# Kernel optimization log

Measured on AMD Instinct MI355X. Metric: run time of the kernel, lower is better.

The kernel has to match this reference:

```python
import jax, jax.numpy as jnp
import numpy as np

B, T, D, H, OUT, VOCAB = 64, 100, 1024, 1024, 28, 28


def setup_inputs() -> dict:
    key = jax.random.key(0)
    ks = jax.random.split(key, 12)
    s = 0.05
    return {
        "x": jax.random.normal(ks[0], (B, T, D), jnp.float32),
        # encoder GRU (keras reset_after=True): kernel [D,3H], recurrent [H,3H], bias [2,3H]
        "enc_W": jax.random.normal(ks[1], (D, 3 * H), jnp.float32) * s,
        "enc_U": jax.random.normal(ks[2], (H, 3 * H), jnp.float32) * s,
        "enc_b": jax.random.normal(ks[3], (2, 3 * H), jnp.float32) * s,
        # AdditiveAttention learned scale vector [H]
        "att_scale": jax.random.normal(ks[4], (H,), jnp.float32) * s,
        # Embedding(28, H)
        "emb_W": jax.random.normal(ks[5], (VOCAB, H), jnp.float32) * s,
        # decoder GRUCell
        "dec_W": jax.random.normal(ks[6], (H, 3 * H), jnp.float32) * s,
        "dec_U": jax.random.normal(ks[7], (H, 3 * H), jnp.float32) * s,
        "dec_b": jax.random.normal(ks[8], (2, 3 * H), jnp.float32) * s,
        # fc: Dense(OUT) on concat([h, context]) -> [2H, OUT]
        "fc_W": jax.random.normal(ks[9], (2 * H, OUT), jnp.float32) * s,
        "fc_b": jax.random.normal(ks[10], (OUT,), jnp.float32) * s,
    }


def _gru_update(x_t, h, W, U, b):
    # keras GRU math with reset_after=True
    mx = x_t @ W + b[0]          # [B,3H]
    mi = h @ U + b[1]            # [B,3H]
    xz, xr, xh = jnp.split(mx, 3, axis=-1)
    rz, rr, rh = jnp.split(mi, 3, axis=-1)
    z = jax.nn.sigmoid(xz + rz)
    r = jax.nn.sigmoid(xr + rr)
    hh = jnp.tanh(xh + r * rh)
    return z * h + (1.0 - z) * hh


def reference(x, enc_W, enc_U, enc_b, att_scale, emb_W, dec_W, dec_U, dec_b, fc_W, fc_b):
    b, t, _ = x.shape
    h = jnp.zeros((b, enc_U.shape[0]), x.dtype)

    # encoder GRU, return_sequences=True
    def enc_step(h, x_t):
        h = _gru_update(x_t, h, enc_W, enc_U, enc_b)
        return h, h

    _, hpe = jax.lax.scan(enc_step, h, jnp.swapaxes(x, 0, 1))  # [T,B,H]
    hpe = jnp.swapaxes(hpe, 0, 1)                              # [B,T,H]

    out_dim = fc_b.shape[0]
    p0 = jnp.zeros((b, out_dim), x.dtype)
    h0 = jnp.zeros((b, dec_U.shape[0]), x.dtype)

    def dec_step(carry, _):
        p, hd = carry
        # additive attention: scores[b,j] = sum_d scale[d]*tanh(q[b,d]+k[b,j,d])
        scores = jnp.einsum('bth,h->bt', jnp.tanh(hd[:, None, :] + hpe), att_scale)
        attn = jax.nn.softmax(scores, axis=-1)
        ctx = jnp.einsum('bt,bth->bh', attn, hpe)
        idx = jnp.argmax(p, axis=-1)          # [B] int
        e = emb_W[idx]                        # [B,H]
        hd = _gru_update(e, hd, dec_W, dec_U, dec_b)
        p = jnp.concatenate([hd, ctx], axis=1) @ fc_W + fc_b
        return (p, hd), p

    _, outs = jax.lax.scan(dec_step, (p0, h0), None, length=t)  # [T,B,OUT]
    return jnp.swapaxes(outs, 0, 1)                              # [B,T,OUT]
```

## Files before the change

### kernel.cpp

```cpp
#include <hip/hip_runtime.h>

#define TT 100
#define HH 1024
#define H3 3072
#define NOUT 28

#define AGENT __HIP_MEMORY_SCOPE_AGENT
#define WGRP  __HIP_MEMORY_SCOPE_WORKGROUP
#define SPIN_CAP (1u<<20)

__device__ __forceinline__ float frcp_(float x){ return __builtin_amdgcn_rcpf(x); }
__device__ __forceinline__ float fsig_(float x){ return frcp_(1.0f + __expf(-x)); }
__device__ __forceinline__ float ftanh_(float x){ return 1.0f - 2.0f*frcp_(__expf(2.0f*x) + 1.0f); }
__device__ __forceinline__ void wait_vm(){ asm volatile("s_waitcnt vmcnt(0)" ::: "memory"); }

__device__ __forceinline__ float4 ld_dev16(const float* p){
    float4 v;
    asm volatile("global_load_dwordx4 %0, %1, off sc0 sc1" : "=v"(v) : "v"(p) : "memory");
    return v;
}
__device__ __forceinline__ unsigned aload4(const int* p){
    return (unsigned)__hip_atomic_load(p, __ATOMIC_RELAXED, AGENT);
}

__device__ __forceinline__ void gridbar(int* slot, int sub, int target){
    __syncthreads();
    if (threadIdx.x == 0){
        __hip_atomic_fetch_add(slot + sub*16, 1, __ATOMIC_RELAXED, AGENT);
        unsigned gy = 0; int s;
        do {
            s = 0;
            #pragma unroll
            for (int c=0;c<16;c++) s += __hip_atomic_load(slot + c*16, __ATOMIC_RELAXED, AGENT);
            if (s < target){ if (++gy > SPIN_CAP) break; __builtin_amdgcn_s_sleep(1); }
        } while (s < target);
    }
    __syncthreads();
}

__device__ __forceinline__ void wbar4(int* c, int tgt){
    asm volatile("s_waitcnt lgkmcnt(0)" ::: "memory");
    if ((threadIdx.x & 63) == 0) __hip_atomic_fetch_add(c, 1, __ATOMIC_RELAXED, WGRP);
    unsigned gy = 0;
    while (__hip_atomic_load(c, __ATOMIC_RELAXED, WGRP) < tgt){ if (++gy > SPIN_CAP) break; }
    asm volatile("" ::: "memory");
}

__global__ void k_init(int* ib, int n){
    int g = blockIdx.x*256 + threadIdx.x;
    if (g < n) ib[g] = 0;
}

__global__ __launch_bounds__(256) void k_transpose(const float* __restrict__ U0,
                                                   const float* __restrict__ U1,
                                                   float* __restrict__ T0,
                                                   float* __restrict__ T1){
    const float* U = blockIdx.z ? U1 : U0;
    float*       T = blockIdx.z ? T1 : T0;
    __shared__ float tile[32][33];
    int tx = threadIdx.x & 31, ty = threadIdx.x >> 5;
    int j0 = blockIdx.x*32, k0 = blockIdx.y*32;
    #pragma unroll
    for (int q=0;q<4;q++){
        int kr = ty + q*8;
        tile[kr][tx] = U[(size_t)(k0+kr)*H3 + j0 + tx];
    }
    __syncthreads();
    #pragma unroll
    for (int q=0;q<4;q++){
        int jr = ty + q*8;
        T[(size_t)(j0+jr)*HH + k0 + tx] = tile[tx][jr];
    }
}

__global__ __launch_bounds__(256) void k_edec(const float* __restrict__ emb,
                                              const float* __restrict__ W,
                                              const float* __restrict__ b0,
                                              float* __restrict__ E){
    int gid = blockIdx.x*256 + threadIdx.x;
    int v = gid / H3, j = gid - v*H3;
    float acc = b0[j];
    const float* er = emb + (size_t)v*HH;
    #pragma unroll 4
    for (int k=0;k<HH;k++) acc = fmaf(er[k], W[(size_t)k*H3 + j], acc);
    E[gid] = acc;
}

__global__ __launch_bounds__(256) void k_mxgemm(const float* __restrict__ A,
                                                const float* __restrict__ W,
                                                const float* __restrict__ b0,
                                                float* __restrict__ MXT){
    __shared__ float aT[32*68];
    __shared__ float bL[32*68];
    int tid = threadIdx.x;
    int row0 = blockIdx.y*64, col0 = blockIdx.x*64;
    int arow = tid>>2, acs = (tid&3)*4;
    int bk   = tid>>3, bcs = (tid&7)*4;
    int ty = tid>>4, tx = tid&15;
    float acc[4][4] = {};
    for (int kk=0; kk<HH; kk+=32){
        #pragma unroll
        for (int i=0;i<2;i++){
            int c = acs + i*16;
            float4 v = *(const float4*)(A + (size_t)(row0+arow)*HH + kk + c);
            aT[(c+0)*68 + arow] = v.x; aT[(c+1)*68 + arow] = v.y;
            aT[(c+2)*68 + arow] = v.z; aT[(c+3)*68 + arow] = v.w;
        }
        #pragma unroll
        for (int i=0;i<2;i++){
            int c = bcs + i*32;
            float4 v = *(const float4*)(W + (size_t)(kk+bk)*H3 + col0 + c);
            *(float4*)(bL + bk*68 + c) = v;
        }
        __syncthreads();
        #pragma unroll
        for (int k=0;k<32;k++){
            float4 a4 = *(const float4*)(aT + k*68 + ty*4);
            float4 b4 = *(const float4*)(bL + k*68 + tx*4);
            acc[0][0]=fmaf(a4.x,b4.x,acc[0][0]); acc[0][1]=fmaf(a4.x,b4.y,acc[0][1]);
            acc[0][2]=fmaf(a4.x,b4.z,acc[0][2]); acc[0][3]=fmaf(a4.x,b4.w,acc[0][3]);
            acc[1][0]=fmaf(a4.y,b4.x,acc[1][0]); acc[1][1]=fmaf(a4.y,b4.y,acc[1][1]);
            acc[1][2]=fmaf(a4.y,b4.z,acc[1][2]); acc[1][3]=fmaf(a4.y,b4.w,acc[1][3]);
            acc[2][0]=fmaf(a4.z,b4.x,acc[2][0]); acc[2][1]=fmaf(a4.z,b4.y,acc[2][1]);
            acc[2][2]=fmaf(a4.z,b4.z,acc[2][2]); acc[2][3]=fmaf(a4.z,b4.w,acc[2][3]);
            acc[3][0]=fmaf(a4.w,b4.x,acc[3][0]); acc[3][1]=fmaf(a4.w,b4.y,acc[3][1]);
            acc[3][2]=fmaf(a4.w,b4.z,acc[3][2]); acc[3][3]=fmaf(a4.w,b4.w,acc[3][3]);
        }
        __syncthreads();
    }
    float4 bb = *(const float4*)(b0 + col0 + tx*4);
    #pragma unroll
    for (int i=0;i<4;i++){
        int r = row0 + ty*4 + i;
        int bq = r / 100; int tq = r - bq*100;
        float v0 = acc[i][0] + bb.x, v1 = acc[i][1] + bb.y;
        float v2 = acc[i][2] + bb.z, v3 = acc[i][3] + bb.w;
        float* dst = MXT + ((size_t)tq*H3 + col0 + tx*4)*64 + bq;
        dst[0]   = v0; dst[64]  = v1; dst[128] = v2; dst[192] = v3;
    }
}

__global__ __launch_bounds__(256) void k_enc(const float* __restrict__ MXT,
                                             const float* __restrict__ Ut,
                                             const float* __restrict__ b1,
                                             float* __restrict__ hpe,
                                             float* __restrict__ hT,
                                             int* __restrict__ bar){
    __shared__ float hs[2][16384];
    int tid = threadIdx.x, lane = tid & 63;
    int wg = blockIdx.x;
    int sub = wg & 15;
    int cu = __builtin_amdgcn_readfirstlane(wg*4 + (tid>>6));
    const float* Uz = Ut + (size_t)cu*HH;
    const float* Ur = Uz + (size_t)HH*HH;
    const float* Uh = Ur + (size_t)HH*HH;
    float bz = b1[cu], br = b1[cu+HH], bh = b1[cu+2*HH];
    for (int t=0; t<TT; ++t){
        int cur = t & 1;
        const float* mx = MXT + (size_t)t*H3*64;
        float xz = mx[(size_t)cu*64 + lane];
        float xr = mx[(size_t)(cu+HH)*64 + lane];
        float xh = mx[(size_t)(cu+2*HH)*64 + lane];
        float az=0.f, ar=0.f, ah=0.f, hp=0.f;
        if (t > 0){
            const float* gq = hT + (size_t)cur*65536;
            float4 sv[16];
            #pragma unroll
            for (int s=0;s<16;s++) sv[s] = ld_dev16(gq + 4*(size_t)(s*256 + tid));
            wait_vm();
            #pragma unroll
            for (int s=0;s<16;s++) ((float4*)hs[0])[s*256 + tid] = sv[s];
            __syncthreads();
            for (int q=0;q<4;++q){
                if (q<3){
                    #pragma unroll
                    for (int s=0;s<16;s++) sv[s] = ld_dev16(gq + (size_t)(q+1)*16384 + 4*(size_t)(s*256 + tid));
                }
                const float* hb = hs[q&1];
                const float* Uzq = Uz + q*256;
                const float* Urq = Ur + q*256;
                const float* Uhq = Uh + q*256;
                #pragma unroll 8
                for (int k=0;k<256;++k){
                    float h = hb[k*64 + lane];
                    az = fmaf(h, Uzq[k], az);
                    ar = fmaf(h, Urq[k], ar);
                    ah = fmaf(h, Uhq[k], ah);
                }
                if ((cu>>8) == q) hp = hb[(cu&255)*64 + lane];
                if (q<3){
                    wait_vm();
                    #pragma unroll
                    for (int s=0;s<16;s++) ((float4*)hs[(q+1)&1])[s*256 + tid] = sv[s];
                }
                __syncthreads();
            }
        }
        float z  = fsig_(xz + az + bz);
        float r  = fsig_(xr + ar + br);
        float hh = ftanh_(xh + r*(ah + bh));
        float hnew = z*hp + (1.f - z)*hh;
        __hip_atomic_store(hT + (size_t)(cur^1)*65536 + cu*64 + lane, hnew, __ATOMIC_RELAXED, AGENT);
        hpe[((size_t)lane*TT + t)*HH + cu] = hnew;
        gridbar(bar + (size_t)t*256, sub, 256);
    }
}

__global__ __launch_bounds__(512) void k_dec(const float* __restrict__ hpe,
                                             const float* __restrict__ Ut,
                                             const float* __restrict__ b1,
                                             const float* __restrict__ Edec,
                                             const float* __restrict__ scale,
                                             const float* __restrict__ fcW,
                                             const float* __restrict__ fcb,
                                             float* __restrict__ hdT,
                                             float* __restrict__ hdl,
                                             float* __restrict__ out,
                                             int* __restrict__ idx_t,
                                             int* __restrict__ bar,
                                             int* __restrict__ flagidx){
    __shared__ float hs[2][16384];
    __shared__ float ctxs[4][1024];
    __shared__ float m_s[4], S_s[4];
    __shared__ int c_a, c_fc, go, cstg;
    int tid = threadIdx.x, wg = blockIdx.x;
    if (tid == 0){ c_a=0; c_fc=0; go=0; cstg=0; }
    __syncthreads();

    if (tid < 256){
        int lane = tid & 63;
        int sub = wg & 15;
        int cu = __builtin_amdgcn_readfirstlane(wg*4 + (tid>>6));
        const float* Uz = Ut + (size_t)cu*HH;
        const float* Ur = Uz + (size_t)HH*HH;
        const float* Uh = Ur + (size_t)HH*HH;
        float bz = b1[cu], br = b1[cu+HH], bh = b1[cu+2*HH];
        int stgt = 0;
        for (int i=0; i<TT; ++i){
            int cur = i & 1;
            float az=0.f, ar=0.f, ah=0.f, hp=0.f;
            if (i > 0){
                const float* gq = hdT + (size_t)cur*65536;
                float4 sv[16];
                #pragma unroll
                for (int s=0;s<16;s++) sv[s] = ld_dev16(gq + 4*(size_t)(s*256 + tid));
                wait_vm();
                #pragma unroll
                for (int s=0;s<16;s++) ((float4*)hs[0])[s*256 + tid] = sv[s];
                wbar4(&cstg, stgt += 4);
                for (int q=0;q<4;++q){
                    if (q<3){
                        #pragma unroll
                        for (int s=0;s<16;s++) sv[s] = ld_dev16(gq + (size_t)(q+1)*16384 + 4*(size_t)(s*256 + tid));
                    }
                    const float* hb = hs[q&1];
                    const float* Uzq = Uz + q*256;
                    const float* Urq = Ur + q*256;
                    const float* Uhq = Uh + q*256;
                    #pragma unroll 8
                    for (int k=0;k<256;++k){
                        float h = hb[k*64 + lane];
                        az = fmaf(h, Uzq[k], az);
                        ar = fmaf(h, Urq[k], ar);
                        ah = fmaf(h, Uhq[k], ah);
                    }
                    if ((cu>>8) == q) hp = hb[(cu&255)*64 + lane];
                    if (q<3){
                        wait_vm();
                        #pragma unroll
                        for (int s=0;s<16;s++) ((float4*)hs[(q+1)&1])[s*256 + tid] = sv[s];
                    }
                    wbar4(&cstg, stgt += 4);
                }
            }
            if (tid == 0){
                unsigned gy = 0; int s;
                do {
                    s = 0;
                    #pragma unroll
                    for (int c=0;c<8;c++) s += __hip_atomic_load(flagidx + (size_t)i*128 + c*16, __ATOMIC_RELAXED, AGENT);
                    if (s < 64){ if (++gy > SPIN_CAP) break; __builtin_amdgcn_s_sleep(1); }
                } while (s < 64);
                __hip_atomic_store(&go, i+1, __ATOMIC_RELAXED, WGRP);
            }
            { unsigned gy=0; while (__hip_atomic_load(&go, __ATOMIC_RELAXED, WGRP) < i+1){ if (++gy > SPIN_CAP) break; } }
            asm volatile("" ::: "memory");
            unsigned mi = aload4(idx_t + (size_t)i*64 + lane);
            if (mi > 27u) mi = 0;
            const float* ed = Edec + (size_t)mi*H3;
            float xz = ed[cu], xr = ed[cu+HH], xh = ed[cu+2*HH];
            float z  = fsig_(xz + az + bz);
            float r  = fsig_(xr + ar + br);
            float hh = ftanh_(xh + r*(ah + bh));
            float hnew = z*hp + (1.f - z)*hh;
            __hip_atomic_store(hdT + (size_t)(cur^1)*65536 + cu*64 + lane, hnew, __ATOMIC_RELAXED, AGENT);
            __hip_atomic_store(hdl + (size_t)(cur^1)*65536 + (size_t)lane*HH + cu, hnew, __ATOMIC_RELAXED, AGENT);
            gridbar(bar + (size_t)i*256, sub, 256);
        }
    } else if (wg < 64){
        int t2 = tid - 256;
        int w = t2 >> 6, lane = t2 & 63, b = wg;
        float sc[16];
        #pragma unroll
        for (int s4=0;s4<4;s4++){
            float4 v = *(const float4*)(scale + lane*16 + s4*4);
            sc[s4*4+0]=v.x; sc[s4*4+1]=v.y; sc[s4*4+2]=v.z; sc[s4*4+3]=v.w;
        }
        int j0 = w*25;
        for (int i=0; i<TT; ++i){
            float q[16];
            if (i == 0){
                #pragma unroll
                for (int d=0;d<16;d++) q[d]=0.f;
            } else {
                const float* hq = hdl + (size_t)(i&1)*65536 + (size_t)b*HH + lane*16;
                float4 q0 = ld_dev16(hq), q1 = ld_dev16(hq+4), q2 = ld_dev16(hq+8), q3 = ld_dev16(hq+12);
                wait_vm();
                q[0]=q0.x;q[1]=q0.y;q[2]=q0.z;q[3]=q0.w;
                q[4]=q1.x;q[5]=q1.y;q[6]=q1.z;q[7]=q1.w;
                q[8]=q2.x;q[9]=q2.y;q[10]=q2.z;q[11]=q2.w;
                q[12]=q3.x;q[13]=q3.y;q[14]=q3.z;q[15]=q3.w;
            }
            if (w == 0){
                if (i > 0){
                    float acc[NOUT];
                    #pragma unroll
                    for (int o=0;o<NOUT;o++) acc[o]=0.f;
                    float cv[16];
                    #pragma unroll
                    for (int s4=0;s4<4;s4++){
                        float4 c0 = ((const float4*)ctxs[0])[lane*4+s4];
                        float4 c1 = ((const float4*)ctxs[1])[lane*4+s4];
                        float4 c2 = ((const float4*)ctxs[2])[lane*4+s4];
                        float4 c3 = ((const float4*)ctxs[3])[lane*4+s4];
                        cv[s4*4+0]=c0.x+c1.x+c2.x+c3.x;
                        cv[s4*4+1]=c0.y+c1.y+c2.y+c3.y;
                        cv[s4*4+2]=c0.z+c1.z+c2.z+c3.z;
                        cv[s4*4+3]=c0.w+c1.w+c2.w+c3.w;
                    }
                    #pragma unroll
                    for (int dd=0;dd<16;++dd){
                        int d = lane*16 + dd;
                        const float* w0p = fcW + (size_t)d*NOUT;
                        const float* w1p = fcW + (size_t)(d+HH)*NOUT;
                        float hv=q[dd], cvv=cv[dd];
                        #pragma unroll
                        for (int o=0;o<NOUT;o++) acc[o] = fmaf(hv, w0p[o], fmaf(cvv, w1p[o], acc[o]));
                    }
                    #pragma unroll
                    for (int o=0;o<NOUT;o++){
                        #pragma unroll
                        for (int m=1;m<64;m<<=1) acc[o] += __shfl_xor(acc[o], m);
                    }
                    float bv=-3.0e38f; int bi=0;
                    #pragma unroll
                    for (int o=0;o<NOUT;o++){
                        float p = acc[o] + fcb[o];
                        acc[o] = p;
                        if (p > bv){ bv = p; bi = o; }
                    }
                    float vout = 0.f;
                    #pragma unroll
                    for (int o=0;o<NOUT;o++) if (lane == o) vout = acc[o];
                    if (lane < NOUT) out[((size_t)b*TT + (i-1))*NOUT + lane] = vout;
                    if (lane == 0){
                        __hip_atomic_store(idx_t + (size_t)i*64 + b, bi, __ATOMIC_RELAXED, AGENT);
                        asm volatile("s_waitcnt vmcnt(0)" ::: "memory");
                    }
                }
                if (lane == 0){
                    __hip_atomic_fetch_add(flagidx + (size_t)i*128 + (b&7)*16, 1, __ATOMIC_RELAXED, AGENT);
                    __hip_atomic_fetch_add(&c_fc, 1, __ATOMIC_RELAXED, WGRP);
                }
            }
            float m = -3.0e38f, S = 0.f;
            float a[16];
            #pragma unroll
            for (int d=0;d<16;d++) a[d]=0.f;
            for (int jj=0;jj<25;jj++){
                int j = j0 + jj;
                const float* hpj = hpe + ((size_t)b*TT + j)*HH + lane*16;
                float va[16];
                {
                    float4 v0 = *(const float4*)(hpj);
                    float4 v1 = *(const float4*)(hpj+4);
                    float4 v2 = *(const float4*)(hpj+8);
                    float4 v3 = *(const float4*)(hpj+12);
                    va[0]=v0.x;va[1]=v0.y;va[2]=v0.z;va[3]=v0.w;
                    va[4]=v1.x;va[5]=v1.y;va[6]=v1.z;va[7]=v1.w;
                    va[8]=v2.x;va[9]=v2.y;va[10]=v2.z;va[11]=v2.w;
                    va[12]=v3.x;va[13]=v3.y;va[14]=v3.z;va[15]=v3.w;
                }
                float s = 0.f;
                #pragma unroll
                for (int d=0;d<16;d++) s += sc[d]*ftanh_(q[d] + va[d]);
                #pragma unroll
                for (int mm=1;mm<64;mm<<=1) s += __shfl_xor(s, mm);
                float mn = fmaxf(m, s);
                float fold = __expf(m - mn);
                float e = __expf(s - mn);
                S = S*fold + e;
                #pragma unroll
                for (int d=0;d<16;d++) a[d] = a[d]*fold + e*va[d];
                m = mn;
            }
            if (lane == 0){ m_s[w] = m; S_s[w] = S; }
            asm volatile("s_waitcnt lgkmcnt(0)" ::: "memory");
            if (lane == 0) __hip_atomic_fetch_add(&c_a, 1, __ATOMIC_RELAXED, WGRP);
            { unsigned gy=0; while (__hip_atomic_load(&c_a, __ATOMIC_RELAXED, WGRP) < 4*(i+1)){ if (++gy > SPIN_CAP) break; } }
            asm volatile("" ::: "memory");
            float M = fmaxf(fmaxf(m_s[0],m_s[1]), fmaxf(m_s[2],m_s[3]));
            float St = S_s[0]*__expf(m_s[0]-M) + S_s[1]*__expf(m_s[1]-M)
                     + S_s[2]*__expf(m_s[2]-M) + S_s[3]*__expf(m_s[3]-M);
            float g = __expf(m - M) * frcp_(St);
            { unsigned gy=0; while (__hip_atomic_load(&c_fc, __ATOMIC_RELAXED, WGRP) < i+1){ if (++gy > SPIN_CAP) break; } }
            asm volatile("" ::: "memory");
            #pragma unroll
            for (int s4=0;s4<4;s4++){
                float4 o4;
                o4.x=a[s4*4+0]*g; o4.y=a[s4*4+1]*g;
                o4.z=a[s4*4+2]*g; o4.w=a[s4*4+3]*g;
                ((float4*)ctxs[w])[lane*4 + s4] = o4;
            }
            gridbar(bar + (size_t)i*256, wg & 15, 256);
        }
        if (w == 0){
            const float* hq = hdl + (size_t)b*HH + lane*16;
            float4 q0 = ld_dev16(hq), q1 = ld_dev16(hq+4), q2 = ld_dev16(hq+8), q3 = ld_dev16(hq+12);
            wait_vm();
            float q[16];
            q[0]=q0.x;q[1]=q0.y;q[2]=q0.z;q[3]=q0.w;
            q[4]=q1.x;q[5]=q1.y;q[6]=q1.z;q[7]=q1.w;
            q[8]=q2.x;q[9]=q2.y;q[10]=q2.z;q[11]=q2.w;
            q[12]=q3.x;q[13]=q3.y;q[14]=q3.z;q[15]=q3.w;
            float acc[NOUT];
            #pragma unroll
            for (int o=0;o<NOUT;o++) acc[o]=0.f;
            float cv[16];
            #pragma unroll
            for (int s4=0;s4<4;s4++){
                float4 c0 = ((const float4*)ctxs[0])[lane*4+s4];
                float4 c1 = ((const float4*)ctxs[1])[lane*4+s4];
                float4 c2 = ((const float4*)ctxs[2])[lane*4+s4];
                float4 c3 = ((const float4*)ctxs[3])[lane*4+s4];
                cv[s4*4+0]=c0.x+c1.x+c2.x+c3.x;
                cv[s4*4+1]=c0.y+c1.y+c2.y+c3.y;
                cv[s4*4+2]=c0.z+c1.z+c2.z+c3.z;
                cv[s4*4+3]=c0.w+c1.w+c2.w+c3.w;
            }
            #pragma unroll
            for (int dd=0;dd<16;++dd){
                int d = lane*16 + dd;
                const float* w0p = fcW + (size_t)d*NOUT;
                const float* w1p = fcW + (size_t)(d+HH)*NOUT;
                float hv=q[dd], cvv=cv[dd];
                #pragma unroll
                for (int o=0;o<NOUT;o++) acc[o] = fmaf(hv, w0p[o], fmaf(cvv, w1p[o], acc[o]));
            }
            #pragma unroll
            for (int o=0;o<NOUT;o++){
                #pragma unroll
                for (int m=1;m<64;m<<=1) acc[o] += __shfl_xor(acc[o], m);
            }
            float vout = 0.f;
            #pragma unroll
            for (int o=0;o<NOUT;o++) if (lane == o) vout = acc[o] + fcb[o];
            if (lane < NOUT) out[((size_t)b*TT + 99)*NOUT + lane] = vout;
        }
    } else {
        for (int i=0;i<TT;++i) gridbar(bar + (size_t)i*256, wg & 15, 256);
    }
}

extern "C" void kernel_launch(void* const* d_in, const int* in_sizes, int n_in,
                              void* d_out, int out_size, void* d_ws, size_t ws_size,
                              hipStream_t stream){
    (void)in_sizes; (void)n_in; (void)out_size; (void)ws_size;
    const float* x     = (const float*)d_in[0];
    const float* encW  = (const float*)d_in[1];
    const float* encU  = (const float*)d_in[2];
    const float* encb  = (const float*)d_in[3];
    const float* scale = (const float*)d_in[4];
    const float* emb   = (const float*)d_in[5];
    const float* decW  = (const float*)d_in[6];
    const float* decU  = (const float*)d_in[7];
    const float* decb  = (const float*)d_in[8];
    const float* fcW   = (const float*)d_in[9];
    const float* fcb   = (const float*)d_in[10];
    float* out = (float*)d_out;
    float* ws  = (float*)d_ws;

    float* MXT   = ws;
    float* hdT   = MXT;
    float* hdl   = MXT + 131072;
    float* encUt = MXT   + 19660800;
    float* decUt = encUt + 3145728;
    float* hpe   = decUt + 3145728;
    float* Edec  = hpe   + 6553600;
    float* hT    = Edec  + 86016;
    int*   ib    = (int*)(hT + 131072);
    int*   bar_enc = ib;
    int*   bar_dec = ib + 25600;
    int*   flagidx = ib + 51200;
    int*   idx_t   = ib + 64000;

    const float* encb1 = encb + H3;
    const float* decb1 = decb + H3;

    k_init<<<276,256,0,stream>>>(ib, 70400);
    k_transpose<<<dim3(96,32,2),256,0,stream>>>(encU, decU, encUt, decUt);
    k_edec<<<336,256,0,stream>>>(emb, decW, decb, Edec);
    k_mxgemm<<<dim3(48,100),256,0,stream>>>(x, encW, encb, MXT);
    k_enc<<<256,256,0,stream>>>(MXT, encUt, encb1, hpe, hT, bar_enc);
    k_dec<<<256,512,0,stream>>>(hpe, decUt, decb1, Edec, scale, fcW, fcb,
                                hdT, hdl, out, idx_t, bar_dec, flagidx);
}
```

Before: 10.22 ms.

## Cache decoder embedding slices in LDS, prefetch attention keys, tweak barrier sleeps

```diff
diff --git a/kernel.cpp b/kernel.cpp
--- a/kernel.cpp
+++ b/kernel.cpp
@@ -18,6 +18,14 @@
     float4 v;
     asm volatile("global_load_dwordx4 %0, %1, off sc0 sc1" : "=v"(v) : "v"(p) : "memory");
     return v;
+}
+__device__ __forceinline__ int ld_dev4i(const int* p){
+    int v;
+    asm volatile("global_load_dword %0, %1, off sc0 sc1" : "=v"(v) : "v"(p) : "memory");
+    return v;
+}
+__device__ __forceinline__ void st_dev4(float* p, float v){
+    asm volatile("global_store_dword %0, %1, off sc0 sc1" :: "v"(p), "v"(v) : "memory");
 }
 __device__ __forceinline__ unsigned aload4(const int* p){
     return (unsigned)__hip_atomic_load(p, __ATOMIC_RELAXED, AGENT);
@@ -32,7 +40,7 @@
             s = 0;
             #pragma unroll
             for (int c=0;c<16;c++) s += __hip_atomic_load(slot + c*16, __ATOMIC_RELAXED, AGENT);
-            if (s < target){ if (++gy > SPIN_CAP) break; __builtin_amdgcn_s_sleep(1); }
+            if (s < target){ if (++gy > SPIN_CAP) break; __builtin_amdgcn_s_sleep(4); }
         } while (s < target);
     }
     __syncthreads();
@@ -200,7 +208,7 @@
         float r  = fsig_(xr + ar + br);
         float hh = ftanh_(xh + r*(ah + bh));
         float hnew = z*hp + (1.f - z)*hh;
-        __hip_atomic_store(hT + (size_t)(cur^1)*65536 + cu*64 + lane, hnew, __ATOMIC_RELAXED, AGENT);
+        st_dev4(hT + (size_t)(cur^1)*65536 + cu*64 + lane, hnew);
         hpe[((size_t)lane*TT + t)*HH + cu] = hnew;
         gridbar(bar + (size_t)t*256, sub, 256);
     }
@@ -221,6 +229,7 @@
                                              int* __restrict__ flagidx){
     __shared__ float hs[2][16384];
     __shared__ float ctxs[4][1024];
+    __shared__ float edl[4][3][28];
     __shared__ float m_s[4], S_s[4];
     __shared__ int c_a, c_fc, go, cstg;
     int tid = threadIdx.x, wg = blockIdx.x;
@@ -230,11 +239,16 @@
     if (tid < 256){
         int lane = tid & 63;
         int sub = wg & 15;
-        int cu = __builtin_amdgcn_readfirstlane(wg*4 + (tid>>6));
+        int wv = tid >> 6;
+        int cu = __builtin_amdgcn_readfirstlane(wg*4 + wv);
         const float* Uz = Ut + (size_t)cu*HH;
         const float* Ur = Uz + (size_t)HH*HH;
         const float* Uh = Ur + (size_t)HH*HH;
         float bz = b1[cu], br = b1[cu+HH], bh = b1[cu+2*HH];
+        for (int tq = lane; tq < 84; tq += 64){
+            int g = tq / 28, v = tq - g*28;
+            edl[wv][g][v] = Edec[(size_t)v*H3 + cu + g*HH];
+        }
         int stgt = 0;
         for (int i=0; i<TT; ++i){
             int cur = i & 1;
@@ -279,22 +293,25 @@
                     s = 0;
                     #pragma unroll
                     for (int c=0;c<8;c++) s += __hip_atomic_load(flagidx + (size_t)i*128 + c*16, __ATOMIC_RELAXED, AGENT);
-                    if (s < 64){ if (++gy > SPIN_CAP) break; __builtin_amdgcn_s_sleep(1); }
+                    if (s < 64){ if (++gy > SPIN_CAP) break; __builtin_amdgcn_s_sleep(4); }
                 } while (s < 64);
                 __hip_atomic_store(&go, i+1, __ATOMIC_RELAXED, WGRP);
             }
             { unsigned gy=0; while (__hip_atomic_load(&go, __ATOMIC_RELAXED, WGRP) < i+1){ if (++gy > SPIN_CAP) break; } }
             asm volatile("" ::: "memory");
-            unsigned mi = aload4(idx_t + (size_t)i*64 + lane);
+            int mi_raw = ld_dev4i(idx_t + (size_t)i*64 + lane);
+            wait_vm();
+            unsigned mi = (unsigned)mi_raw;
             if (mi > 27u) mi = 0;
-            const float* ed = Edec + (size_t)mi*H3;
-            float xz = ed[cu], xr = ed[cu+HH], xh = ed[cu+2*HH];
+            float xz = edl[wv][0][mi];
+            float xr = edl[wv][1][mi];
+            float xh = edl[wv][2][mi];
             float z  = fsig_(xz + az + bz);
             float r  = fsig_(xr + ar + br);
             float hh = ftanh_(xh + r*(ah + bh));
             float hnew = z*hp + (1.f - z)*hh;
-            __hip_atomic_store(hdT + (size_t)(cur^1)*65536 + cu*64 + lane, hnew, __ATOMIC_RELAXED, AGENT);
-            __hip_atomic_store(hdl + (size_t)(cur^1)*65536 + (size_t)lane*HH + cu, hnew, __ATOMIC_RELAXED, AGENT);
+            st_dev4(hdT + (size_t)(cur^1)*65536 + cu*64 + lane, hnew);
+            st_dev4(hdl + (size_t)(cur^1)*65536 + (size_t)lane*HH + cu, hnew);
             gridbar(bar + (size_t)i*256, sub, 256);
         }
     } else if (wg < 64){
@@ -307,6 +324,7 @@
             sc[s4*4+0]=v.x; sc[s4*4+1]=v.y; sc[s4*4+2]=v.z; sc[s4*4+3]=v.w;
         }
         int j0 = w*25;
+        const float* hpb = hpe + ((size_t)b*TT + j0)*HH + lane*16;
         for (int i=0; i<TT; ++i){
             float q[16];
             if (i == 0){
@@ -377,20 +395,24 @@
             float a[16];
             #pragma unroll
             for (int d=0;d<16;d++) a[d]=0.f;
+            float4 n0 = *(const float4*)(hpb);
+            float4 n1 = *(const float4*)(hpb+4);
+            float4 n2 = *(const float4*)(hpb+8);
+            float4 n3 = *(const float4*)(hpb+12);
             for (int jj=0;jj<25;jj++){
-                int j = j0 + jj;
-                const float* hpj = hpe + ((size_t)b*TT + j)*HH + lane*16;
+                float4 v0=n0, v1=n1, v2=n2, v3=n3;
+                if (jj < 24){
+                    const float* hpn = hpb + (size_t)(jj+1)*HH;
+                    n0 = *(const float4*)(hpn);
+                    n1 = *(const float4*)(hpn+4);
+                    n2 = *(const float4*)(hpn+8);
+                    n3 = *(const float4*)(hpn+12);
+                }
                 float va[16];
-                {
-                    float4 v0 = *(const float4*)(hpj);
-                    float4 v1 = *(const float4*)(hpj+4);
-                    float4 v2 = *(const float4*)(hpj+8);
-                    float4 v3 = *(const float4*)(hpj+12);
-                    va[0]=v0.x;va[1]=v0.y;va[2]=v0.z;va[3]=v0.w;
-                    va[4]=v1.x;va[5]=v1.y;va[6]=v1.z;va[7]=v1.w;
-                    va[8]=v2.x;va[9]=v2.y;va[10]=v2.z;va[11]=v2.w;
-                    va[12]=v3.x;va[13]=v3.y;va[14]=v3.z;va[15]=v3.w;
-                }
+                va[0]=v0.x;va[1]=v0.y;va[2]=v0.z;va[3]=v0.w;
+                va[4]=v1.x;va[5]=v1.y;va[6]=v1.z;va[7]=v1.w;
+                va[8]=v2.x;va[9]=v2.y;va[10]=v2.z;va[11]=v2.w;
+                va[12]=v3.x;va[13]=v3.y;va[14]=v3.z;va[15]=v3.w;
                 float s = 0.f;
                 #pragma unroll
                 for (int d=0;d<16;d++) s += sc[d]*ftanh_(q[d] + va[d]);
```

After: 10.14 ms. Within noise of the previous version (-0.8%).
